# Kernel optimization log

Hardware: AMD Instinct MI355X
Metric: run time of the kernel (lower is better)

## Reference

```python
import math
import jax, jax.numpy as jnp
import numpy as np

D_MODEL = 4096
N_Q_HEADS = 32
N_KV_HEADS = 8
HEAD_DIM = D_MODEL // N_Q_HEADS  # 128
N_GROUPS = N_Q_HEADS // N_KV_HEADS  # 4
B, S = 1, 2048


def setup_inputs() -> dict:
    key = jax.random.key(0)
    k1, k2, k3, k4, k5 = jax.random.split(key, 5)
    scale = 1.0 / math.sqrt(D_MODEL)
    return {
        "x": jax.random.normal(k1, (B, S, D_MODEL), dtype=jnp.float32),
        "W_q": jax.random.normal(k2, (N_Q_HEADS * HEAD_DIM, D_MODEL), dtype=jnp.float32) * scale,
        "W_k": jax.random.normal(k3, (N_KV_HEADS * HEAD_DIM, D_MODEL), dtype=jnp.float32) * scale,
        "W_v": jax.random.normal(k4, (N_KV_HEADS * HEAD_DIM, D_MODEL), dtype=jnp.float32) * scale,
        "W_o": jax.random.normal(k5, (D_MODEL, D_MODEL), dtype=jnp.float32) * scale,
    }


def reference(x, W_q, W_k, W_v, W_o):
    Bsz, Sq, _ = x.shape
    # projections (nn.Linear, no bias): y = x @ W.T
    q = (x @ W_q.T).reshape(Bsz, Sq, N_Q_HEADS, HEAD_DIM).transpose(0, 2, 1, 3)   # [B,Hq,S,d]
    k = (x @ W_k.T).reshape(Bsz, Sq, N_KV_HEADS, HEAD_DIM).transpose(0, 2, 1, 3)  # [B,Hkv,S,d]
    v = (x @ W_v.T).reshape(Bsz, Sq, N_KV_HEADS, HEAD_DIM).transpose(0, 2, 1, 3)
    # physical KV head repeat (repeat_interleave over head dim)
    k_rep = jnp.repeat(k, N_GROUPS, axis=1)  # [B,Hq,S,d]
    v_rep = jnp.repeat(v, N_GROUPS, axis=1)
    scores = jnp.einsum("bhqd,bhkd->bhqk", q, k_rep) / math.sqrt(HEAD_DIM)
    attn = jax.nn.softmax(scores, axis=-1)  # no causal mask in the original
    out = jnp.einsum("bhqk,bhkd->bhqd", attn, v_rep)
    out = out.transpose(0, 2, 1, 3).reshape(Bsz, Sq, D_MODEL)
    out = out @ W_o.T
    # original returns first n_kv_heads slices of the REPEATED k/v as the "cache"
    return out, (k_rep[:, :N_KV_HEADS], v_rep[:, :N_KV_HEADS])
```

## Files before the change

kernel.cpp:

```cpp
#include <hip/hip_runtime.h>
#include <hip/hip_bf16.h>

typedef __bf16 bf16;
typedef float f32x4 __attribute__((ext_vector_type(4)));
typedef float f32x16 __attribute__((ext_vector_type(16)));
typedef bf16 bf16x8 __attribute__((ext_vector_type(8)));
typedef bf16 bf16x2 __attribute__((ext_vector_type(2)));
typedef unsigned u32x4 __attribute__((ext_vector_type(4)));

#define MFMA16(a,b,c) __builtin_amdgcn_mfma_f32_16x16x32_bf16((a),(b),(c),0,0,0)
#define MFMA32(a,b,c) __builtin_amdgcn_mfma_f32_32x32x16_bf16((a),(b),(c),0,0,0)

__device__ __forceinline__ void gload16(const void* g, void* l) {
    __builtin_amdgcn_global_load_lds((const __attribute__((address_space(1))) unsigned*)g,
                                     (__attribute__((address_space(3))) unsigned*)l, 16, 0, 0);
}

__device__ __forceinline__ unsigned pk(float lo, float hi) {
    bf16x2 t; t[0] = (bf16)lo; t[1] = (bf16)hi;
    return __builtin_bit_cast(unsigned, t);
}

__device__ __forceinline__ void cvt8(const float* __restrict__ in, bf16* __restrict__ out, int i) {
    const float4* p = (const float4*)in + (size_t)i * 2;
    float4 a = p[0], b = p[1];
    bf16x8 o;
    o[0]=(bf16)a.x; o[1]=(bf16)a.y; o[2]=(bf16)a.z; o[3]=(bf16)a.w;
    o[4]=(bf16)b.x; o[5]=(bf16)b.y; o[6]=(bf16)b.z; o[7]=(bf16)b.w;
    *((bf16x8*)out + i) = o;
}

__global__ __launch_bounds__(256) void cvt_all(const float* __restrict__ x, const float* __restrict__ wq,
                                               const float* __restrict__ wk, const float* __restrict__ wv,
                                               bf16* __restrict__ xb, bf16* __restrict__ wqkv) {
    int i = blockIdx.x * 256 + threadIdx.x;
    const float* src; bf16* dst; int n8;
    switch (blockIdx.y) {
        case 0: src = x;  dst = xb;                 n8 = 1048576; break;
        case 1: src = wq; dst = wqkv;               n8 = 2097152; break;
        case 2: src = wk; dst = wqkv + 16777216;    n8 = 524288;  break;
        default: src = wv; dst = wqkv + 20971520;   n8 = 524288;  break;
    }
    if (i < n8) cvt8(src, dst, i);
}

__global__ __launch_bounds__(256) void cvt_one(const float* __restrict__ in, bf16* __restrict__ out, int n8) {
    int i = blockIdx.x * 256 + threadIdx.x;
    if (i < n8) cvt8(in, out, i);
}

__device__ __forceinline__ void gemm_core(const bf16* __restrict__ A, const bf16* __restrict__ B,
                                          int K, int bm, int bn, bf16* As, bf16* Bs, f32x4 (&acc)[4][4]) {
    const int tid = threadIdx.x, lane = tid & 63, wv = tid >> 6;
    const int wr = wv >> 1, wc = wv & 1, lr = lane & 15, ls = lane >> 4;

#pragma unroll
    for (int mm=0;mm<4;++mm)
#pragma unroll
        for (int nn=0;nn<4;++nn)
#pragma unroll
            for (int r=0;r<4;++r) acc[mm][nn][r] = 0.f;

    for (int k0 = 0; k0 < K; k0 += 64) {
        __syncthreads();
#pragma unroll
        for (int i=0;i<4;++i) {
            int off = i*4096 + wv*1024 + lane*16;
            int row = off >> 7;
            int cg = (lane & 7) ^ (row & 7);
            gload16(A + (size_t)(bm+row)*K + k0 + cg*8, (char*)As + i*4096 + wv*1024);
        }
#pragma unroll
        for (int i=0;i<4;++i) {
            int off = i*4096 + wv*1024 + lane*16;
            int row = off >> 7;
            int cg = (lane & 7) ^ (row & 7);
            gload16(B + (size_t)(bn+row)*K + k0 + cg*8, (char*)Bs + i*4096 + wv*1024);
        }
        __syncthreads();

#pragma unroll
        for (int ks=0; ks<2; ++ks) {
            bf16x8 af[4], bfr[4];
#pragma unroll
            for (int mm=0;mm<4;++mm) {
                int row = wr*64 + mm*16 + lr;
                af[mm] = *(const bf16x8*)((char*)As + row*128 + (((ks*4+ls) ^ (row&7))<<4));
            }
#pragma unroll
            for (int nn=0;nn<4;++nn) {
                int row = wc*64 + nn*16 + lr;
                bfr[nn] = *(const bf16x8*)((char*)Bs + row*128 + (((ks*4+ls) ^ (row&7))<<4));
            }
#pragma unroll
            for (int mm=0;mm<4;++mm)
#pragma unroll
                for (int nn=0;nn<4;++nn) acc[mm][nn] = MFMA16(af[mm], bfr[nn], acc[mm][nn]);
        }
    }
}

__global__ __launch_bounds__(256) void gemm_qkv(const bf16* __restrict__ A, const bf16* __restrict__ W,
                                                bf16* __restrict__ C, float qscale) {
    __shared__ __align__(16) bf16 As[128*64];
    __shared__ __align__(16) bf16 Bs[128*64];
    int flat = blockIdx.y * gridDim.x + blockIdx.x;
    int id = (flat & 7) * 96 + (flat >> 3);
    int bm = (id & 15) * 128, bn = (id >> 4) * 128;
    f32x4 acc[4][4];
    gemm_core(A, W, 4096, bm, bn, As, Bs, acc);

    const float s = (bn < 4096) ? qscale : 1.0f;
    const int lane = threadIdx.x & 63, wv = threadIdx.x >> 6;
    const int wr = wv >> 1, wc = wv & 1, lr = lane & 15, ls = lane >> 4;
#pragma unroll
    for (int mm=0;mm<4;++mm)
#pragma unroll
        for (int nn=0;nn<4;++nn)
#pragma unroll
            for (int r=0;r<4;++r) {
                int mg = bm + wr*64 + mm*16 + ls*4 + r;
                int ng = bn + wc*64 + nn*16 + lr;
                C[(size_t)mg * 6144 + ng] = (bf16)(acc[mm][nn][r] * s);
            }
}

__global__ __launch_bounds__(256) void gemm_o(const bf16* __restrict__ A, const bf16* __restrict__ B,
                                              float* __restrict__ Cp) {
    __shared__ __align__(16) bf16 As[128*64];
    __shared__ __align__(16) bf16 Bs[128*64];
    int flat = blockIdx.y * gridDim.x + blockIdx.x;
    int id = (flat & 7) * 64 + (flat >> 3);
    int bm = (id & 15) * 128, bn = (id >> 4) * 128;
    f32x4 acc[4][4];
    gemm_core(A, B, 4096, bm, bn, As, Bs, acc);

    const int lane = threadIdx.x & 63, wv = threadIdx.x >> 6;
    const int wr = wv >> 1, wc = wv & 1, lr = lane & 15, ls = lane >> 4;
#pragma unroll
    for (int mm=0;mm<4;++mm)
#pragma unroll
        for (int nn=0;nn<4;++nn)
#pragma unroll
            for (int r=0;r<4;++r) {
                int mg = bm + wr*64 + mm*16 + ls*4 + r;
                int ng = bn + wc*64 + nn*16 + lr;
                Cp[(size_t)mg * 4096 + ng] = acc[mm][nn][r];
            }
}

__global__ __launch_bounds__(256) void trans_cache(const bf16* __restrict__ QKVb, bf16* __restrict__ Vt,
                                                   float* __restrict__ cacheK, float* __restrict__ cacheV) {
    int b = blockIdx.x;
    if (b < 512) {
        __shared__ bf16 t[64][70];
        int dt = b & 15, st = b >> 4;
        int tt = threadIdx.x;
        int r = tt >> 2, c0 = (tt & 3) * 16;
#pragma unroll
        for (int i = 0; i < 2; ++i) {
            bf16x8 v = *(const bf16x8*)(QKVb + (size_t)(st*64 + r)*6144 + 5120 + dt*64 + c0 + i*8);
#pragma unroll
            for (int j = 0; j < 8; ++j) t[c0 + i*8 + j][r] = v[j];
        }
        __syncthreads();
        int c = tt >> 2, r0 = (tt & 3) * 16;
#pragma unroll
        for (int i = 0; i < 2; ++i) {
            bf16x8 v = *(const bf16x8*)(&t[c][r0 + i*8]);
            *(bf16x8*)(Vt + (size_t)(dt*64 + c)*2048 + st*64 + r0 + i*8) = v;
        }
    } else {
        int g = (b - 512) * 256 + threadIdx.x;
        int d8 = g & 15, s = (g >> 4) & 2047, j = (g >> 15) & 7, kv = g >> 18;
        int hk = j >> 2;
        bf16x8 v = *(const bf16x8*)(QKVb + (size_t)s*6144 + 4096 + kv*1024 + hk*128 + d8*8);
        float* dst = (kv ? cacheV : cacheK) + ((size_t)j*2048 + s)*128 + d8*8;
        float4 lo, hi;
        lo.x=(float)v[0]; lo.y=(float)v[1]; lo.z=(float)v[2]; lo.w=(float)v[3];
        hi.x=(float)v[4]; hi.y=(float)v[5]; hi.z=(float)v[6]; hi.w=(float)v[7];
        *(float4*)dst = lo;
        *(float4*)(dst + 4) = hi;
    }
}

__device__ __forceinline__ void stage_kv(const bf16* __restrict__ QKVb, const bf16* __restrict__ Vt,
                                         char* Ks, char* Vs, int kvh, int kt, int buf,
                                         int wv, int lane) {
#pragma unroll
    for (int i=0;i<2;++i) {
        int off = i*8192 + wv*1024 + lane*16;
        int row = off >> 8;
        int cg = (lane & 15) ^ (row & 7);
        gload16(QKVb + (size_t)(kt*64+row)*6144 + 4096 + kvh*128 + cg*8, Ks + buf*16384 + i*8192 + wv*1024);
    }
#pragma unroll
    for (int i=0;i<2;++i) {
        int off = i*8192 + wv*1024 + lane*16;
        int d = off >> 7;
        int cg = (lane & 7) ^ (d & 7);
        gload16(Vt + (size_t)(kvh*128+d)*2048 + kt*64 + cg*8, Vs + buf*16384 + i*8192 + wv*1024);
    }
}

__global__ __launch_bounds__(512) void flash_attn(const bf16* __restrict__ QKVb, const bf16* __restrict__ Vt,
                                                  bf16* __restrict__ AO) {
    __shared__ __align__(16) char Ks[2*16384];
    __shared__ __align__(16) char Vs[2*16384];
    const int tid = threadIdx.x, lane = tid & 63, wq = tid >> 6;
    const int l31 = lane & 31, hi = lane >> 5;
    const int h = blockIdx.y, kvh = h >> 2;
    const int q0w = blockIdx.x * 256 + wq * 32;

    bf16x8 qf[8];
#pragma unroll
    for (int f=0; f<8; ++f)
        qf[f] = *(const bf16x8*)(QKVb + (size_t)(q0w + l31)*6144 + h*128 + f*16 + hi*8);

    f32x16 acc[4];
#pragma unroll
    for (int db=0;db<4;++db)
#pragma unroll
        for (int r=0;r<16;++r) acc[db][r] = 0.f;
    float mrun = -1e30f, lrun = 0.f;

    stage_kv(QKVb, Vt, Ks, Vs, kvh, 0, 0, wq, lane);
    __syncthreads();

    for (int t = 0; t < 32; ++t) {
        const int cur = t & 1;
        if (t + 1 < 32) stage_kv(QKVb, Vt, Ks, Vs, kvh, t+1, cur^1, wq, lane);

        const char* KsB = Ks + cur*16384;
        f32x16 sc[2];
#pragma unroll
        for (int kc=0;kc<2;++kc)
#pragma unroll
            for (int r=0;r<16;++r) sc[kc][r] = 0.f;
#pragma unroll
        for (int f=0; f<8; ++f) {
            int r0 = l31, r1 = 32 + l31;
            bf16x8 k0 = *(const bf16x8*)(KsB + r0*256 + (((f*2+hi) ^ (r0&7))<<4));
            bf16x8 k1 = *(const bf16x8*)(KsB + r1*256 + (((f*2+hi) ^ (r1&7))<<4));
            sc[0] = MFMA32(k0, qf[f], sc[0]);
            sc[1] = MFMA32(k1, qf[f], sc[1]);
        }

        float tmax = sc[0][0];
#pragma unroll
        for (int r=1;r<16;++r) tmax = fmaxf(tmax, sc[0][r]);
#pragma unroll
        for (int r=0;r<16;++r) tmax = fmaxf(tmax, sc[1][r]);
        tmax = fmaxf(tmax, __shfl_xor(tmax, 32, 64));
        if (!__all(tmax <= mrun + 8.f)) {
            float mnew = fmaxf(mrun, tmax);
            float corr = __expf(mrun - mnew);
            mrun = mnew;
            lrun *= corr;
#pragma unroll
            for (int r=0;r<16;++r) {
                float cr = __shfl(corr, (r&3) + 8*(r>>2) + 4*hi, 64);
#pragma unroll
                for (int db=0;db<4;++db) acc[db][r] *= cr;
            }
        }
        float rs = 0.f;
#pragma unroll
        for (int kc=0;kc<2;++kc)
#pragma unroll
            for (int r=0;r<16;++r) { float e = __expf(sc[kc][r] - mrun); sc[kc][r] = e; rs += e; }
        rs += __shfl_xor(rs, 32, 64);
        lrun += rs;

        bf16x8 pa[4];
#pragma unroll
        for (int kb=0;kb<4;++kb) {
            const int kc = kb>>1, r0 = (kb&1)*8;
            unsigned a0 = pk(sc[kc][r0+0], sc[kc][r0+1]);
            unsigned a1 = pk(sc[kc][r0+2], sc[kc][r0+3]);
            unsigned b0 = pk(sc[kc][r0+4], sc[kc][r0+5]);
            unsigned b1 = pk(sc[kc][r0+6], sc[kc][r0+7]);
            unsigned sa0 = (unsigned)__shfl_xor((int)a0, 32, 64);
            unsigned sa1 = (unsigned)__shfl_xor((int)a1, 32, 64);
            unsigned sb0 = (unsigned)__shfl_xor((int)b0, 32, 64);
            unsigned sb1 = (unsigned)__shfl_xor((int)b1, 32, 64);
            u32x4 w;
            w[0] = hi ? sb0 : a0;
            w[1] = hi ? sb1 : a1;
            w[2] = hi ? b0 : sa0;
            w[3] = hi ? b1 : sa1;
            pa[kb] = __builtin_bit_cast(bf16x8, w);
        }

        const char* VsB = Vs + cur*16384;
#pragma unroll
        for (int db=0;db<4;++db) {
            const int d = db*32 + l31;
#pragma unroll
            for (int kb=0;kb<4;++kb) {
                bf16x8 vf = *(const bf16x8*)(VsB + d*128 + (((kb*2+hi) ^ (d&7))<<4));
                acc[db] = MFMA32(pa[kb], vf, acc[db]);
            }
        }
        __syncthreads();
    }

    float linv = 1.0f / lrun;
#pragma unroll
    for (int r=0;r<16;++r) {
        int crw = (r&3) + 8*(r>>2) + 4*hi;
        float lv = __shfl(linv, crw, 64);
        size_t qrow = (size_t)q0w + crw;
#pragma unroll
        for (int db=0;db<4;++db)
            AO[qrow*4096 + h*128 + db*32 + l31] = (bf16)(acc[db][r] * lv);
    }
}

extern "C" void kernel_launch(void* const* d_in, const int* in_sizes, int n_in,
                              void* d_out, int out_size, void* d_ws, size_t ws_size,
                              hipStream_t stream) {
    const float* x  = (const float*)d_in[0];
    const float* Wq = (const float*)d_in[1];
    const float* Wk = (const float*)d_in[2];
    const float* Wv = (const float*)d_in[3];
    const float* Wo = (const float*)d_in[4];

    bf16* xb   = (bf16*)d_ws;
    bf16* QKVb = xb + (size_t)8388608;
    bf16* Wqkv = QKVb + (size_t)12582912;
    bf16* Vt  = xb;
    bf16* Wob = Wqkv;
    bf16* AO  = Wqkv + (size_t)16777216;

    float* out = (float*)d_out;
    float* cacheK = out + (size_t)8388608;
    float* cacheV = cacheK + (size_t)2097152;

    const float qscale = 0.08838834764831845f;

    cvt_all<<<dim3(8192, 4), 256, 0, stream>>>(x, Wq, Wk, Wv, xb, Wqkv);
    gemm_qkv<<<dim3(16, 48), 256, 0, stream>>>(xb, Wqkv, QKVb, qscale);
    cvt_one<<<8192, 256, 0, stream>>>(Wo, Wob, 2097152);
    trans_cache<<<2560, 256, 0, stream>>>(QKVb, Vt, cacheK, cacheV);
    flash_attn<<<dim3(8, 32), 512, 0, stream>>>(QKVb, Vt, AO);
    gemm_o<<<dim3(16, 32), 256, 0, stream>>>(AO, Wob, out);
}
```

Baseline: 361.6 us.

## Double-buffer GEMM LDS tiles with K=32 prefetch of next tile

Restructures the shared GEMM main loop to use two LDS buffers with a K-step of 32, issuing the async global-to-LDS loads for the next tile before running MFMAs on the current one. This reduces to one barrier per iteration and aims to hide global load latency behind compute. The swizzle is adapted to 64-byte rows. The trade-off is fewer MFMAs per barrier and a shallow prefetch distance that depends on the barrier's waitcnt for correctness.

```diff
diff --git a/kernel.cpp b/kernel.cpp
--- a/kernel.cpp
+++ b/kernel.cpp
@@ -49,6 +49,19 @@
     if (i < n8) cvt8(in, out, i);
 }
 
+__device__ __forceinline__ void stage_tile(const bf16* __restrict__ A, const bf16* __restrict__ B,
+                                           int K, int bm, int bn, int k0,
+                                           bf16* As, bf16* Bs, int wv, int lane) {
+#pragma unroll
+    for (int i=0;i<2;++i) {
+        int off = i*4096 + wv*1024 + lane*16;
+        int row = off >> 6;
+        int cg  = (lane & 3) ^ ((row >> 1) & 3);
+        gload16(A + (size_t)(bm+row)*K + k0 + cg*8, (char*)As + off);
+        gload16(B + (size_t)(bn+row)*K + k0 + cg*8, (char*)Bs + off);
+    }
+}
+
 __device__ __forceinline__ void gemm_core(const bf16* __restrict__ A, const bf16* __restrict__ B,
                                           int K, int bm, int bn, bf16* As, bf16* Bs, f32x4 (&acc)[4][4]) {
     const int tid = threadIdx.x, lane = tid & 63, wv = tid >> 6;
@@ -61,49 +74,41 @@
 #pragma unroll
             for (int r=0;r<4;++r) acc[mm][nn][r] = 0.f;
 
-    for (int k0 = 0; k0 < K; k0 += 64) {
+    const int nt = K >> 5;
+    stage_tile(A, B, K, bm, bn, 0, As, Bs, wv, lane);
+    __syncthreads();
+
+    for (int t = 0; t < nt; ++t) {
+        const int cur = t & 1;
+        bf16* AsC = As + cur * 4096;
+        bf16* BsC = Bs + cur * 4096;
+        if (t + 1 < nt)
+            stage_tile(A, B, K, bm, bn, (t+1) << 5, As + (cur^1)*4096, Bs + (cur^1)*4096, wv, lane);
+
+        bf16x8 af[4], bfr[4];
+#pragma unroll
+        for (int mm=0;mm<4;++mm) {
+            int row = wr*64 + mm*16 + lr;
+            af[mm] = *(const bf16x8*)((char*)AsC + row*64 + ((ls ^ ((row>>1)&3))<<4));
+        }
+#pragma unroll
+        for (int nn=0;nn<4;++nn) {
+            int row = wc*64 + nn*16 + lr;
+            bfr[nn] = *(const bf16x8*)((char*)BsC + row*64 + ((ls ^ ((row>>1)&3))<<4));
+        }
+#pragma unroll
+        for (int mm=0;mm<4;++mm)
+#pragma unroll
+            for (int nn=0;nn<4;++nn) acc[mm][nn] = MFMA16(af[mm], bfr[nn], acc[mm][nn]);
+
         __syncthreads();
-#pragma unroll
-        for (int i=0;i<4;++i) {
-            int off = i*4096 + wv*1024 + lane*16;
-            int row = off >> 7;
-            int cg = (lane & 7) ^ (row & 7);
-            gload16(A + (size_t)(bm+row)*K + k0 + cg*8, (char*)As + i*4096 + wv*1024);
-        }
-#pragma unroll
-        for (int i=0;i<4;++i) {
-            int off = i*4096 + wv*1024 + lane*16;
-            int row = off >> 7;
-            int cg = (lane & 7) ^ (row & 7);
-            gload16(B + (size_t)(bn+row)*K + k0 + cg*8, (char*)Bs + i*4096 + wv*1024);
-        }
-        __syncthreads();
-
-#pragma unroll
-        for (int ks=0; ks<2; ++ks) {
-            bf16x8 af[4], bfr[4];
-#pragma unroll
-            for (int mm=0;mm<4;++mm) {
-                int row = wr*64 + mm*16 + lr;
-                af[mm] = *(const bf16x8*)((char*)As + row*128 + (((ks*4+ls) ^ (row&7))<<4));
-            }
-#pragma unroll
-            for (int nn=0;nn<4;++nn) {
-                int row = wc*64 + nn*16 + lr;
-                bfr[nn] = *(const bf16x8*)((char*)Bs + row*128 + (((ks*4+ls) ^ (row&7))<<4));
-            }
-#pragma unroll
-            for (int mm=0;mm<4;++mm)
-#pragma unroll
-                for (int nn=0;nn<4;++nn) acc[mm][nn] = MFMA16(af[mm], bfr[nn], acc[mm][nn]);
-        }
     }
 }
 
 __global__ __launch_bounds__(256) void gemm_qkv(const bf16* __restrict__ A, const bf16* __restrict__ W,
                                                 bf16* __restrict__ C, float qscale) {
-    __shared__ __align__(16) bf16 As[128*64];
-    __shared__ __align__(16) bf16 Bs[128*64];
+    __shared__ __align__(16) bf16 As[2*128*32];
+    __shared__ __align__(16) bf16 Bs[2*128*32];
     int flat = blockIdx.y * gridDim.x + blockIdx.x;
     int id = (flat & 7) * 96 + (flat >> 3);
     int bm = (id & 15) * 128, bn = (id >> 4) * 128;
@@ -127,8 +132,8 @@
 
 __global__ __launch_bounds__(256) void gemm_o(const bf16* __restrict__ A, const bf16* __restrict__ B,
                                               float* __restrict__ Cp) {
-    __shared__ __align__(16) bf16 As[128*64];
-    __shared__ __align__(16) bf16 Bs[128*64];
+    __shared__ __align__(16) bf16 As[2*128*32];
+    __shared__ __align__(16) bf16 Bs[2*128*32];
     int flat = blockIdx.y * gridDim.x + blockIdx.x;
     int id = (flat & 7) * 64 + (flat >> 3);
     int bm = (id & 15) * 128, bn = (id >> 4) * 128;
```

Result: slower. 382.1 us (+5.7%).
